# Optimization experiments

Measured on AMD Instinct MI355X. Metric: run time of the kernel, lower is better.

## Reference

```python
import jax, jax.numpy as jnp
import numpy as np
import math

HEADS = 4
LN_EPS = 1e-5


def _layer_norm(x, gamma, beta):
    # LayerNorm over last dim (N=4096), matching nn.LayerNorm(4096)
    mu = jnp.mean(x, axis=-1, keepdims=True)
    var = jnp.mean((x - mu) ** 2, axis=-1, keepdims=True)
    return (x - mu) * jax.lax.rsqrt(var + LN_EPS) * gamma + beta


def setup_inputs() -> dict:
    key = jax.random.key(0)
    ks = jax.random.split(key, 10)
    L, IMG, N = 1024, 1024, 4096
    s_img = 1.0 / math.sqrt(IMG)
    s_L = 1.0 / math.sqrt(L)
    return {
        "point_features": jax.random.normal(ks[0], (1, L, N), jnp.float32),
        "img_features": jax.random.normal(ks[1], (1, IMG, N), jnp.float32),
        # 4 per-head 1x1 convs IMG_chl -> L_chl
        "W_img": jax.random.normal(ks[2], (HEADS, L, IMG), jnp.float32) * s_img,
        "b_img": jax.random.normal(ks[3], (HEADS, L), jnp.float32) * s_img,
        # conv_L: L_chl -> L_chl
        "W_L": jax.random.normal(ks[4], (L, L), jnp.float32) * s_L,
        "b_L": jax.random.normal(ks[5], (L,), jnp.float32) * s_L,
        # LayerNorm(4096)
        "ln_g": jnp.ones((N,), jnp.float32),
        "ln_b": jnp.zeros((N,), jnp.float32),
        # conv_fusion: L_chl -> L_chl
        "W_f": jax.random.normal(ks[6], (L, L), jnp.float32) * s_L,
        "b_f": jax.random.normal(ks[7], (L,), jnp.float32) * s_L,
    }


def reference(point_features, img_features, W_img, b_img, W_L, b_L, ln_g, ln_b, W_f, b_f):
    # L_query = conv_L(point_features): [1, L, N]
    L_query = jnp.einsum('oi,bin->bon', W_L, point_features) + b_L[None, :, None]
    dk = L_query.shape[1]
    N = L_query.shape[2]

    # All 4 head keys at once: [H, 1, L, N]
    keys = jnp.einsum('hoi,bin->hbon', W_img, img_features) + b_img[:, None, :, None]

    # score_i = sum_c(key_i * query) / sqrt(dk)  -> cat over heads: [H, N] (B=1)
    score = jnp.sum(keys * L_query[None], axis=2).reshape(HEADS, N) / jnp.sqrt(jnp.float32(dk))

    # softmax across heads (dim=0), weightmap = [1, H, N]
    weight = jax.nn.softmax(score, axis=0)
    weightmap = weight[None]

    # z = sum_h weight[h] * key_h : [1, L, N]
    z = jnp.einsum('hn,hbcn->bcn', weight, keys)

    fused = _layer_norm(z + L_query, ln_g, ln_b)
    fusion_features = jnp.einsum('oi,bin->bon', W_f, fused) + b_f[None, :, None]
    return (fusion_features, weightmap)
```

## Files before the change

### kernel.cpp

```cpp
#include <hip/hip_runtime.h>
#include <hip/hip_bf16.h>
#include <stdint.h>

using u16 = unsigned short;

typedef __attribute__((ext_vector_type(8))) short bf16x8;
typedef __attribute__((ext_vector_type(4))) float f32x4;

typedef const __attribute__((address_space(1))) unsigned int* gas_t;
typedef __attribute__((address_space(3))) unsigned int* las_t;

__device__ inline void g2l16(const u16* g, u16* l) {
  __builtin_amdgcn_global_load_lds((gas_t)g, (las_t)l, 16, 0, 0);
}

__device__ inline u16 f2b(float x) {
  union { float f; uint32_t u; } v; v.f = x;
  uint32_t r = (v.u + 0x7FFFu + ((v.u >> 16) & 1u)) >> 16;
  return (u16)r;
}
__device__ inline float b2f(u16 b) {
  union { uint32_t u; float f; } v; v.u = ((uint32_t)b) << 16;
  return v.f;
}
__device__ inline float b2f_lo(uint32_t p) {
  union { uint32_t u; float f; } v; v.u = p << 16; return v.f;
}
__device__ inline float b2f_hi(uint32_t p) {
  union { uint32_t u; float f; } v; v.u = p & 0xFFFF0000u; return v.f;
}

__device__ inline void store_out(float* p, float v) { *p = v; }
__device__ inline void store_out(u16* p, float v) { *p = f2b(v); }

template<typename OutT>
__device__ inline void gemm_tile_128(const u16* __restrict__ A,
                                     const u16* __restrict__ Bt,
                                     const float* __restrict__ bias,
                                     OutT* __restrict__ C,
                                     int m0, int n0, int N, int K,
                                     u16* As, u16* Bs)
{
  const int tid  = threadIdx.x;
  const int wave = tid >> 6;
  const int lane = tid & 63;
  const int wm = wave >> 1, wn = wave & 1;
  const int lr = lane & 15;
  const int lq = lane >> 4;
  const int x7 = lr & 7;

  const int srow = tid >> 3;
  const int sgc  = (tid & 7) ^ (srow & 7);
  const u16* gA = A  + (size_t)(m0 + srow) * K + sgc * 8;
  const u16* gB = Bt + (size_t)(n0 + srow) * K + sgc * 8;
  u16* dstA = As + wave * 512;
  u16* dstB = Bs + wave * 512;

  f32x4 acc[4][4];
  #pragma unroll
  for (int i = 0; i < 4; ++i)
    #pragma unroll
    for (int j = 0; j < 4; ++j)
      acc[i][j] = (f32x4){0.f, 0.f, 0.f, 0.f};

  for (int k0 = 0; k0 < K; k0 += 64) {
    #pragma unroll
    for (int s = 0; s < 4; ++s) {
      g2l16(gA + (size_t)(s * 32) * K + k0, dstA + s * 2048);
      g2l16(gB + (size_t)(s * 32) * K + k0, dstB + s * 2048);
    }
    __syncthreads();

    #pragma unroll
    for (int ks = 0; ks < 2; ++ks) {
      const int pa = (ks * 4 + lq) ^ x7;
      bf16x8 af[4], bfr[4];
      #pragma unroll
      for (int im = 0; im < 4; ++im)
        af[im] = *(const bf16x8*)&As[(wm * 64 + im * 16 + lr) * 64 + pa * 8];
      #pragma unroll
      for (int in = 0; in < 4; ++in)
        bfr[in] = *(const bf16x8*)&Bs[(wn * 64 + in * 16 + lr) * 64 + pa * 8];

      #pragma unroll
      for (int im = 0; im < 4; ++im)
        #pragma unroll
        for (int in = 0; in < 4; ++in)
          acc[im][in] = __builtin_amdgcn_mfma_f32_16x16x32_bf16(
              af[im], bfr[in], acc[im][in], 0, 0, 0);
    }
    __syncthreads();
  }

  #pragma unroll
  for (int im = 0; im < 4; ++im) {
    const int mbase = m0 + wm * 64 + im * 16 + lq * 4;
    #pragma unroll
    for (int in = 0; in < 4; ++in) {
      const int ncol = n0 + wn * 64 + in * 16 + lr;
      #pragma unroll
      for (int r = 0; r < 4; ++r) {
        const int m = mbase + r;
        store_out(C + (size_t)m * N + ncol, acc[im][in][r] + bias[m]);
      }
    }
  }
}

__global__ __launch_bounds__(256)
void gemm_keys_q(const u16* __restrict__ WIb, const u16* __restrict__ IT,
                 const float* __restrict__ bim, u16* __restrict__ KEYS,
                 const u16* __restrict__ WLb, const u16* __restrict__ PT,
                 const float* __restrict__ bL, u16* __restrict__ Qb)
{
  __shared__ u16 As[128 * 64];
  __shared__ u16 Bs[128 * 64];
  const int by = blockIdx.y;
  const bool keys = (by < 32);
  const u16*   A    = keys ? WIb : WLb;
  const u16*   Bt   = keys ? IT  : PT;
  const float* bias = keys ? bim : bL;
  u16*         C    = keys ? KEYS : Qb;
  const int m0 = (by & 31) * 128;
  const int n0 = blockIdx.x * 128;
  gemm_tile_128<u16>(A, Bt, bias, C, m0, n0, 4096, 1024, As, Bs);
}

template<typename OutT>
__global__ __launch_bounds__(256)
void gemm_bt_64(const u16* __restrict__ A, const u16* __restrict__ Bt,
                const float* __restrict__ bias, OutT* __restrict__ C,
                int M, int N, int K)
{
  __shared__ u16 As[64 * 64];
  __shared__ u16 Bs[128 * 64];

  const int tid  = threadIdx.x;
  const int wave = tid >> 6;
  const int lane = tid & 63;
  const int lr = lane & 15;
  const int lq = lane >> 4;
  const int x7 = lr & 7;

  const int m0 = blockIdx.y * 64;
  const int n0 = blockIdx.x * 128;

  const int srow = tid >> 3;
  const int sgc  = (tid & 7) ^ (srow & 7);
  const u16* gA = A  + (size_t)(m0 + srow) * K + sgc * 8;
  const u16* gB = Bt + (size_t)(n0 + srow) * K + sgc * 8;
  u16* dstA = As + wave * 512;
  u16* dstB = Bs + wave * 512;

  f32x4 acc[4][2];
  #pragma unroll
  for (int i = 0; i < 4; ++i)
    #pragma unroll
    for (int j = 0; j < 2; ++j)
      acc[i][j] = (f32x4){0.f, 0.f, 0.f, 0.f};

  for (int k0 = 0; k0 < K; k0 += 64) {
    #pragma unroll
    for (int s = 0; s < 2; ++s)
      g2l16(gA + (size_t)(s * 32) * K + k0, dstA + s * 2048);
    #pragma unroll
    for (int s = 0; s < 4; ++s)
      g2l16(gB + (size_t)(s * 32) * K + k0, dstB + s * 2048);
    __syncthreads();

    #pragma unroll
    for (int ks = 0; ks < 2; ++ks) {
      const int pa = (ks * 4 + lq) ^ x7;
      bf16x8 af[4], bfr[2];
      #pragma unroll
      for (int im = 0; im < 4; ++im)
        af[im] = *(const bf16x8*)&As[(im * 16 + lr) * 64 + pa * 8];
      #pragma unroll
      for (int in = 0; in < 2; ++in)
        bfr[in] = *(const bf16x8*)&Bs[(wave * 32 + in * 16 + lr) * 64 + pa * 8];

      #pragma unroll
      for (int im = 0; im < 4; ++im)
        #pragma unroll
        for (int in = 0; in < 2; ++in)
          acc[im][in] = __builtin_amdgcn_mfma_f32_16x16x32_bf16(
              af[im], bfr[in], acc[im][in], 0, 0, 0);
    }
    __syncthreads();
  }

  #pragma unroll
  for (int im = 0; im < 4; ++im) {
    const int mbase = m0 + im * 16 + lq * 4;
    #pragma unroll
    for (int in = 0; in < 2; ++in) {
      const int ncol = n0 + wave * 32 + in * 16 + lr;
      #pragma unroll
      for (int r = 0; r < 4; ++r) {
        const int m = mbase + r;
        store_out(C + (size_t)m * N + ncol, acc[im][in][r] + bias[m]);
      }
    }
  }
}

__global__ __launch_bounds__(256)
void prep(const float* __restrict__ P, u16* __restrict__ PT,
          const float* __restrict__ I, u16* __restrict__ IT,
          const float4* __restrict__ wim, const float4* __restrict__ wl,
          const float4* __restrict__ wf, ushort4* __restrict__ wimb,
          ushort4* __restrict__ wlb, ushort4* __restrict__ wfb)
{
  const int bid = blockIdx.x;
  if (bid < 8192) {
    const int z   = bid >> 12;
    const int rem = bid & 4095;
    const int bx  = rem & 127;
    const int byy = rem >> 7;
    const float* in = z ? I : P;
    u16* out = z ? IT : PT;
    __shared__ u16 tile[32][33];
    const int c0 = bx * 32, r0 = byy * 32;
    const int tx = threadIdx.x & 31, ty = threadIdx.x >> 5;
    #pragma unroll
    for (int k = 0; k < 4; ++k)
      tile[ty + 8 * k][tx] = f2b(in[(size_t)(r0 + ty + 8 * k) * 4096 + c0 + tx]);
    __syncthreads();
    #pragma unroll
    for (int k = 0; k < 4; ++k)
      out[(size_t)(c0 + ty + 8 * k) * 1024 + r0 + tx] = tile[tx][ty + 8 * k];
  } else {
    int i = (bid - 8192) * 256 + threadIdx.x;
    const float4* src; ushort4* dst;
    if (i < 1048576)      { src = wim; dst = wimb; }
    else if (i < 1310720) { src = wl;  dst = wlb;  i -= 1048576; }
    else                  { src = wf;  dst = wfb;  i -= 1310720; }
    const float4 v = src[i];
    ushort4 o;
    o.x = f2b(v.x); o.y = f2b(v.y); o.z = f2b(v.z); o.w = f2b(v.w);
    dst[i] = o;
  }
}

__global__ __launch_bounds__(256)
void transpose_u16(const u16* __restrict__ in, u16* __restrict__ out,
                   int R, int C)
{
  __shared__ u16 tile[32][33];
  const int c0 = blockIdx.x * 32, r0 = blockIdx.y * 32;
  const int tx = threadIdx.x & 31, ty = threadIdx.x >> 5;
  #pragma unroll
  for (int k = 0; k < 4; ++k)
    tile[ty + 8 * k][tx] = in[(size_t)(r0 + ty + 8 * k) * C + c0 + tx];
  __syncthreads();
  #pragma unroll
  for (int k = 0; k < 4; ++k)
    out[(size_t)(c0 + ty + 8 * k) * R + r0 + tx] = tile[tx][ty + 8 * k];
}

__global__ __launch_bounds__(256)
void score_partial(const u16* __restrict__ keys, const u16* __restrict__ Qb,
                   float* __restrict__ score)
{
  const int n  = blockIdx.x * 256 + threadIdx.x;
  const int c0 = blockIdx.y * 32;
  float s[4] = {0.f, 0.f, 0.f, 0.f};
  for (int c = c0; c < c0 + 32; ++c) {
    const float q = b2f(Qb[(size_t)c * 4096 + n]);
    #pragma unroll
    for (int h = 0; h < 4; ++h)
      s[h] = fmaf(q, b2f(keys[((size_t)((h << 10) + c)) * 4096 + n]), s[h]);
  }
  #pragma unroll
  for (int h = 0; h < 4; ++h)
    atomicAdd(&score[h * 4096 + n], s[h] * 0.03125f);
}

__global__ __launch_bounds__(256)
void softmax_h(const float* __restrict__ score, float* __restrict__ wmap)
{
  const int n = blockIdx.x * 256 + threadIdx.x;
  const float s0 = score[n], s1 = score[4096 + n];
  const float s2 = score[8192 + n], s3 = score[12288 + n];
  const float m = fmaxf(fmaxf(s0, s1), fmaxf(s2, s3));
  const float e0 = expf(s0 - m), e1 = expf(s1 - m);
  const float e2 = expf(s2 - m), e3 = expf(s3 - m);
  const float inv = 1.f / (e0 + e1 + e2 + e3);
  wmap[n] = e0 * inv; wmap[4096 + n] = e1 * inv;
  wmap[8192 + n] = e2 * inv; wmap[12288 + n] = e3 * inv;
}

__global__ __launch_bounds__(256)
void z_ln(const u16* __restrict__ keys, const u16* __restrict__ Qb,
          const float* __restrict__ w, const float* __restrict__ g,
          const float* __restrict__ bb, u16* __restrict__ fused)
{
  const int c  = blockIdx.x;
  const int tx = threadIdx.x;
  float t[16];
  float s = 0.f, s2 = 0.f;
  #pragma unroll
  for (int j = 0; j < 2; ++j) {
    const int n = tx * 8 + j * 2048;
    const uint4 qv = *(const uint4*)&Qb[(size_t)c * 4096 + n];
    float z[8] = {0.f,0.f,0.f,0.f,0.f,0.f,0.f,0.f};
    #pragma unroll
    for (int h = 0; h < 4; ++h) {
      const uint4 kv = *(const uint4*)&keys[((size_t)((h << 10) + c)) * 4096 + n];
      const float4 w0 = *(const float4*)&w[h * 4096 + n];
      const float4 w1 = *(const float4*)&w[h * 4096 + n + 4];
      z[0] = fmaf(w0.x, b2f_lo(kv.x), z[0]);
      z[1] = fmaf(w0.y, b2f_hi(kv.x), z[1]);
      z[2] = fmaf(w0.z, b2f_lo(kv.y), z[2]);
      z[3] = fmaf(w0.w, b2f_hi(kv.y), z[3]);
      z[4] = fmaf(w1.x, b2f_lo(kv.z), z[4]);
      z[5] = fmaf(w1.y, b2f_hi(kv.z), z[5]);
      z[6] = fmaf(w1.z, b2f_lo(kv.w), z[6]);
      z[7] = fmaf(w1.w, b2f_hi(kv.w), z[7]);
    }
    const uint32_t qs[4] = {qv.x, qv.y, qv.z, qv.w};
    #pragma unroll
    for (int e = 0; e < 4; ++e) {
      const float v0 = z[2 * e]     + b2f_lo(qs[e]);
      const float v1 = z[2 * e + 1] + b2f_hi(qs[e]);
      t[8 * j + 2 * e]     = v0;
      t[8 * j + 2 * e + 1] = v1;
      s += v0 + v1;
      s2 = fmaf(v0, v0, fmaf(v1, v1, s2));
    }
  }
  #pragma unroll
  for (int o = 32; o > 0; o >>= 1) {
    s  += __shfl_down(s, o);
    s2 += __shfl_down(s2, o);
  }
  __shared__ float rbuf[8];
  const int wave = tx >> 6, lane = tx & 63;
  if (lane == 0) { rbuf[wave] = s; rbuf[4 + wave] = s2; }
  __syncthreads();
  s  = rbuf[0] + rbuf[1] + rbuf[2] + rbuf[3];
  s2 = rbuf[4] + rbuf[5] + rbuf[6] + rbuf[7];
  const float mu  = s * (1.f / 4096.f);
  const float var = s2 * (1.f / 4096.f) - mu * mu;
  const float rs  = rsqrtf(var + 1e-5f);
  #pragma unroll
  for (int j = 0; j < 2; ++j) {
    const int n = tx * 8 + j * 2048;
    #pragma unroll
    for (int q4 = 0; q4 < 2; ++q4) {
      const float4 gv = *(const float4*)&g[n + 4 * q4];
      const float4 bv = *(const float4*)&bb[n + 4 * q4];
      ushort4 o;
      o.x = f2b((t[8 * j + 4 * q4]     - mu) * rs * gv.x + bv.x);
      o.y = f2b((t[8 * j + 4 * q4 + 1] - mu) * rs * gv.y + bv.y);
      o.z = f2b((t[8 * j + 4 * q4 + 2] - mu) * rs * gv.z + bv.z);
      o.w = f2b((t[8 * j + 4 * q4 + 3] - mu) * rs * gv.w + bv.w);
      *(ushort4*)&fused[(size_t)c * 4096 + n + 4 * q4] = o;
    }
  }
}

extern "C" void kernel_launch(void* const* d_in, const int* in_sizes, int n_in,
                              void* d_out, int out_size, void* d_ws, size_t ws_size,
                              hipStream_t stream)
{
  const float* P   = (const float*)d_in[0];
  const float* I   = (const float*)d_in[1];
  const float* Wim = (const float*)d_in[2];
  const float* bim = (const float*)d_in[3];
  const float* WL  = (const float*)d_in[4];
  const float* bL  = (const float*)d_in[5];
  const float* lng = (const float*)d_in[6];
  const float* lnb = (const float*)d_in[7];
  const float* Wf  = (const float*)d_in[8];
  const float* bf_ = (const float*)d_in[9];
  float* out = (float*)d_out;

  char* ws = (char*)d_ws;
  u16*   PT     = (u16*)(ws + 0);
  u16*   IT     = (u16*)(ws + (size_t)8  * 1048576);
  u16*   WLb    = (u16*)(ws + (size_t)16 * 1048576);
  u16*   WIb    = (u16*)(ws + (size_t)18 * 1048576);
  u16*   WFb    = (u16*)(ws + (size_t)26 * 1048576);
  u16*   Qb     = (u16*)(ws + (size_t)28 * 1048576);
  u16*   KEYS   = (u16*)(ws + (size_t)36 * 1048576);
  float* SCORE  = (float*)(ws + (size_t)68 * 1048576);
  u16*   FUSED  = (u16*)(ws + (size_t)70 * 1048576);
  u16*   FUSEDT = (u16*)(ws + (size_t)78 * 1048576);

  const dim3 b256(256);

  prep<<<14336, b256, 0, stream>>>(P, PT, I, IT,
                                   (const float4*)Wim, (const float4*)WL,
                                   (const float4*)Wf, (ushort4*)WIb,
                                   (ushort4*)WLb, (ushort4*)WFb);

  gemm_keys_q<<<dim3(32, 40), b256, 0, stream>>>(WIb, IT, bim, KEYS,
                                                 WLb, PT, bL, Qb);

  hipMemsetAsync(SCORE, 0, 4 * 4096 * sizeof(float), stream);
  score_partial<<<dim3(16, 32), b256, 0, stream>>>(KEYS, Qb, SCORE);
  float* wmap = out + (size_t)1024 * 4096;
  softmax_h<<<16, b256, 0, stream>>>(SCORE, wmap);

  z_ln<<<1024, b256, 0, stream>>>(KEYS, Qb, wmap, lng, lnb, FUSED);
  transpose_u16<<<dim3(128, 32), b256, 0, stream>>>(FUSED, FUSEDT, 1024, 4096);

  gemm_bt_64<float><<<dim3(32, 16), b256, 0, stream>>>(WFb, FUSEDT, bf_, out, 1024, 4096, 1024);
}
```

Before: 212.6 us.

## Vectorize transposes with 64x64 tiles and replace score atomics with partial sums

The fp32->bf16 input transposes and the fused-output transpose now use 64x64 LDS tiles with vector loads and stores instead of 32x32 scalar accesses. The score reduction writes per-channel-block partial sums into a reused workspace region rather than doing atomicAdd onto a memset buffer. The softmax kernel sums the 64 partials. This removes the memset and the atomic contention but adds an extra 4MB partial-buffer read in softmax.

```diff
diff --git a/kernel.cpp b/kernel.cpp
--- a/kernel.cpp
+++ b/kernel.cpp
@@ -212,25 +212,38 @@
           ushort4* __restrict__ wlb, ushort4* __restrict__ wfb)
 {
   const int bid = blockIdx.x;
-  if (bid < 8192) {
-    const int z   = bid >> 12;
-    const int rem = bid & 4095;
-    const int bx  = rem & 127;
-    const int byy = rem >> 7;
+  if (bid < 2048) {
+    const int z   = bid >> 10;
+    const int rem = bid & 1023;
+    const int ct  = rem & 63;
+    const int rt  = rem >> 6;
     const float* in = z ? I : P;
     u16* out = z ? IT : PT;
-    __shared__ u16 tile[32][33];
-    const int c0 = bx * 32, r0 = byy * 32;
-    const int tx = threadIdx.x & 31, ty = threadIdx.x >> 5;
-    #pragma unroll
-    for (int k = 0; k < 4; ++k)
-      tile[ty + 8 * k][tx] = f2b(in[(size_t)(r0 + ty + 8 * k) * 4096 + c0 + tx]);
+    __shared__ u16 tile[64][72];
+    const int r0 = rt * 64, c0 = ct * 64;
+    const int tr  = threadIdx.x >> 4;
+    const int tc4 = threadIdx.x & 15;
+    #pragma unroll
+    for (int it = 0; it < 4; ++it) {
+      const int r = it * 16 + tr;
+      const float4 v = *(const float4*)&in[(size_t)(r0 + r) * 4096 + c0 + tc4 * 4];
+      ushort4 o;
+      o.x = f2b(v.x); o.y = f2b(v.y); o.z = f2b(v.z); o.w = f2b(v.w);
+      *(ushort4*)&tile[r][tc4 * 4] = o;
+    }
     __syncthreads();
     #pragma unroll
-    for (int k = 0; k < 4; ++k)
-      out[(size_t)(c0 + ty + 8 * k) * 1024 + r0 + tx] = tile[tx][ty + 8 * k];
+    for (int it = 0; it < 4; ++it) {
+      const int c = it * 16 + tr;
+      ushort4 o;
+      o.x = tile[tc4 * 4 + 0][c];
+      o.y = tile[tc4 * 4 + 1][c];
+      o.z = tile[tc4 * 4 + 2][c];
+      o.w = tile[tc4 * 4 + 3][c];
+      *(ushort4*)&out[(size_t)(c0 + c) * 1024 + r0 + tc4 * 4] = o;
+    }
   } else {
-    int i = (bid - 8192) * 256 + threadIdx.x;
+    int i = (bid - 2048) * 256 + threadIdx.x;
     const float4* src; ushort4* dst;
     if (i < 1048576)      { src = wim; dst = wimb; }
     else if (i < 1310720) { src = wl;  dst = wlb;  i -= 1048576; }
@@ -246,42 +259,73 @@
 void transpose_u16(const u16* __restrict__ in, u16* __restrict__ out,
                    int R, int C)
 {
-  __shared__ u16 tile[32][33];
-  const int c0 = blockIdx.x * 32, r0 = blockIdx.y * 32;
-  const int tx = threadIdx.x & 31, ty = threadIdx.x >> 5;
-  #pragma unroll
-  for (int k = 0; k < 4; ++k)
-    tile[ty + 8 * k][tx] = in[(size_t)(r0 + ty + 8 * k) * C + c0 + tx];
+  __shared__ u16 tile[64][72];
+  const int c0 = blockIdx.x * 64, r0 = blockIdx.y * 64;
+  const int tr  = threadIdx.x >> 4;
+  const int tc4 = threadIdx.x & 15;
+  #pragma unroll
+  for (int it = 0; it < 4; ++it) {
+    const int r = it * 16 + tr;
+    *(ushort4*)&tile[r][tc4 * 4] =
+        *(const ushort4*)&in[(size_t)(r0 + r) * C + c0 + tc4 * 4];
+  }
   __syncthreads();
   #pragma unroll
-  for (int k = 0; k < 4; ++k)
-    out[(size_t)(c0 + ty + 8 * k) * R + r0 + tx] = tile[tx][ty + 8 * k];
+  for (int it = 0; it < 4; ++it) {
+    const int c = it * 16 + tr;
+    ushort4 o;
+    o.x = tile[tc4 * 4 + 0][c];
+    o.y = tile[tc4 * 4 + 1][c];
+    o.z = tile[tc4 * 4 + 2][c];
+    o.w = tile[tc4 * 4 + 3][c];
+    *(ushort4*)&out[(size_t)(c0 + c) * R + r0 + tc4 * 4] = o;
+  }
 }
 
 __global__ __launch_bounds__(256)
 void score_partial(const u16* __restrict__ keys, const u16* __restrict__ Qb,
-                   float* __restrict__ score)
-{
-  const int n  = blockIdx.x * 256 + threadIdx.x;
-  const int c0 = blockIdx.y * 32;
-  float s[4] = {0.f, 0.f, 0.f, 0.f};
-  for (int c = c0; c < c0 + 32; ++c) {
-    const float q = b2f(Qb[(size_t)c * 4096 + n]);
-    #pragma unroll
-    for (int h = 0; h < 4; ++h)
-      s[h] = fmaf(q, b2f(keys[((size_t)((h << 10) + c)) * 4096 + n]), s[h]);
-  }
+                   float* __restrict__ part)
+{
+  const int n  = blockIdx.x * 1024 + threadIdx.x * 4;
+  const int c0 = blockIdx.y * 16;
+  float s[4][4];
   #pragma unroll
   for (int h = 0; h < 4; ++h)
-    atomicAdd(&score[h * 4096 + n], s[h] * 0.03125f);
-}
-
-__global__ __launch_bounds__(256)
-void softmax_h(const float* __restrict__ score, float* __restrict__ wmap)
+    #pragma unroll
+    for (int e = 0; e < 4; ++e) s[h][e] = 0.f;
+
+  for (int c = c0; c < c0 + 16; ++c) {
+    const uint2 qv = *(const uint2*)&Qb[(size_t)c * 4096 + n];
+    const float q0 = b2f_lo(qv.x), q1 = b2f_hi(qv.x);
+    const float q2 = b2f_lo(qv.y), q3 = b2f_hi(qv.y);
+    #pragma unroll
+    for (int h = 0; h < 4; ++h) {
+      const uint2 kv = *(const uint2*)&keys[((size_t)((h << 10) + c)) * 4096 + n];
+      s[h][0] = fmaf(q0, b2f_lo(kv.x), s[h][0]);
+      s[h][1] = fmaf(q1, b2f_hi(kv.x), s[h][1]);
+      s[h][2] = fmaf(q2, b2f_lo(kv.y), s[h][2]);
+      s[h][3] = fmaf(q3, b2f_hi(kv.y), s[h][3]);
+    }
+  }
+  #pragma unroll
+  for (int h = 0; h < 4; ++h) {
+    float4 o;
+    o.x = s[h][0] * 0.03125f; o.y = s[h][1] * 0.03125f;
+    o.z = s[h][2] * 0.03125f; o.w = s[h][3] * 0.03125f;
+    *(float4*)&part[((size_t)(blockIdx.y * 4 + h)) * 4096 + n] = o;
+  }
+}
+
+__global__ __launch_bounds__(256)
+void softmax_h(const float* __restrict__ part, float* __restrict__ wmap)
 {
   const int n = blockIdx.x * 256 + threadIdx.x;
-  const float s0 = score[n], s1 = score[4096 + n];
-  const float s2 = score[8192 + n], s3 = score[12288 + n];
+  float s0 = 0.f, s1 = 0.f, s2 = 0.f, s3 = 0.f;
+  #pragma unroll 4
+  for (int cy = 0; cy < 64; ++cy) {
+    const float* p = part + (size_t)cy * 16384 + n;
+    s0 += p[0]; s1 += p[4096]; s2 += p[8192]; s3 += p[12288];
+  }
   const float m = fmaxf(fmaxf(s0, s1), fmaxf(s2, s3));
   const float e0 = expf(s0 - m), e1 = expf(s1 - m);
   const float e2 = expf(s2 - m), e3 = expf(s3 - m);
@@ -384,27 +428,26 @@
   u16*   WFb    = (u16*)(ws + (size_t)26 * 1048576);
   u16*   Qb     = (u16*)(ws + (size_t)28 * 1048576);
   u16*   KEYS   = (u16*)(ws + (size_t)36 * 1048576);
-  float* SCORE  = (float*)(ws + (size_t)68 * 1048576);
+  float* PART   = (float*)(ws + 0);
   u16*   FUSED  = (u16*)(ws + (size_t)70 * 1048576);
   u16*   FUSEDT = (u16*)(ws + (size_t)78 * 1048576);
 
   const dim3 b256(256);
 
-  prep<<<14336, b256, 0, stream>>>(P, PT, I, IT,
-                                   (const float4*)Wim, (const float4*)WL,
-                                   (const float4*)Wf, (ushort4*)WIb,
-                                   (ushort4*)WLb, (ushort4*)WFb);
+  prep<<<8192, b256, 0, stream>>>(P, PT, I, IT,
+                                  (const float4*)Wim, (const float4*)WL,
+                                  (const float4*)Wf, (ushort4*)WIb,
+                                  (ushort4*)WLb, (ushort4*)WFb);
 
   gemm_keys_q<<<dim3(32, 40), b256, 0, stream>>>(WIb, IT, bim, KEYS,
                                                  WLb, PT, bL, Qb);
 
-  hipMemsetAsync(SCORE, 0, 4 * 4096 * sizeof(float), stream);
-  score_partial<<<dim3(16, 32), b256, 0, stream>>>(KEYS, Qb, SCORE);
+  score_partial<<<dim3(4, 64), b256, 0, stream>>>(KEYS, Qb, PART);
   float* wmap = out + (size_t)1024 * 4096;
-  softmax_h<<<16, b256, 0, stream>>>(SCORE, wmap);
+  softmax_h<<<16, b256, 0, stream>>>(PART, wmap);
 
   z_ln<<<1024, b256, 0, stream>>>(KEYS, Qb, wmap, lng, lnb, FUSED);
-  transpose_u16<<<dim3(128, 32), b256, 0, stream>>>(FUSED, FUSEDT, 1024, 4096);
+  transpose_u16<<<dim3(64, 16), b256, 0, stream>>>(FUSED, FUSEDT, 1024, 4096);
 
   gemm_bt_64<float><<<dim3(32, 16), b256, 0, stream>>>(WFb, FUSEDT, bf_, out, 1024, 4096, 1024);
 }
```

Measured after the change: 217.8 us. +2.4%, slower.

## Fuse score reduction into key GEMM epilogue, compute query GEMM separately first

Applied to the files above, without the earlier changes.

The query projection now runs first as its own GEMM launch, so the key GEMM epilogue can read the query tile and build the per-head score partial sums directly. The partials are reduced across lanes with shuffles and added atomically. This removes the separate score kernel and its full re-read of the keys tensor. In exchange the query and key GEMMs no longer share one launch, the epilogue does extra global loads of the query values, and there are more atomics on the score buffer.

```diff
diff --git a/kernel.cpp b/kernel.cpp
--- a/kernel.cpp
+++ b/kernel.cpp
@@ -33,13 +33,10 @@
 __device__ inline void store_out(float* p, float v) { *p = v; }
 __device__ inline void store_out(u16* p, float v) { *p = f2b(v); }
 
-template<typename OutT>
-__device__ inline void gemm_tile_128(const u16* __restrict__ A,
+__device__ inline void gemm_core_128(const u16* __restrict__ A,
                                      const u16* __restrict__ Bt,
-                                     const float* __restrict__ bias,
-                                     OutT* __restrict__ C,
-                                     int m0, int n0, int N, int K,
-                                     u16* As, u16* Bs)
+                                     int m0, int n0, int K,
+                                     u16* As, u16* Bs, f32x4 (&acc)[4][4])
 {
   const int tid  = threadIdx.x;
   const int wave = tid >> 6;
@@ -56,7 +53,6 @@
   u16* dstA = As + wave * 512;
   u16* dstB = Bs + wave * 512;
 
-  f32x4 acc[4][4];
   #pragma unroll
   for (int i = 0; i < 4; ++i)
     #pragma unroll
@@ -91,7 +87,29 @@
     }
     __syncthreads();
   }
-
+}
+
+__global__ __launch_bounds__(256)
+void gemm_keys_score(const u16* __restrict__ WIb, const u16* __restrict__ IT,
+                     const float* __restrict__ bim, u16* __restrict__ KEYS,
+                     const u16* __restrict__ Qb, float* __restrict__ score)
+{
+  __shared__ u16 As[128 * 64];
+  __shared__ u16 Bs[128 * 64];
+  const int m0 = blockIdx.y * 128;
+  const int n0 = blockIdx.x * 128;
+  f32x4 acc[4][4];
+  gemm_core_128(WIb, IT, m0, n0, 1024, As, Bs, acc);
+
+  const int tid  = threadIdx.x;
+  const int wave = tid >> 6;
+  const int lane = tid & 63;
+  const int wm = wave >> 1, wn = wave & 1;
+  const int lr = lane & 15;
+  const int lq = lane >> 4;
+  const int h  = m0 >> 10;
+
+  float sp[4] = {0.f, 0.f, 0.f, 0.f};
   #pragma unroll
   for (int im = 0; im < 4; ++im) {
     const int mbase = m0 + wm * 64 + im * 16 + lq * 4;
@@ -101,29 +119,21 @@
       #pragma unroll
       for (int r = 0; r < 4; ++r) {
         const int m = mbase + r;
-        store_out(C + (size_t)m * N + ncol, acc[im][in][r] + bias[m]);
+        const float v = acc[im][in][r] + bim[m];
+        KEYS[(size_t)m * 4096 + ncol] = f2b(v);
+        sp[in] = fmaf(v, b2f(Qb[(size_t)(m & 1023) * 4096 + ncol]), sp[in]);
       }
     }
   }
-}
-
-__global__ __launch_bounds__(256)
-void gemm_keys_q(const u16* __restrict__ WIb, const u16* __restrict__ IT,
-                 const float* __restrict__ bim, u16* __restrict__ KEYS,
-                 const u16* __restrict__ WLb, const u16* __restrict__ PT,
-                 const float* __restrict__ bL, u16* __restrict__ Qb)
-{
-  __shared__ u16 As[128 * 64];
-  __shared__ u16 Bs[128 * 64];
-  const int by = blockIdx.y;
-  const bool keys = (by < 32);
-  const u16*   A    = keys ? WIb : WLb;
-  const u16*   Bt   = keys ? IT  : PT;
-  const float* bias = keys ? bim : bL;
-  u16*         C    = keys ? KEYS : Qb;
-  const int m0 = (by & 31) * 128;
-  const int n0 = blockIdx.x * 128;
-  gemm_tile_128<u16>(A, Bt, bias, C, m0, n0, 4096, 1024, As, Bs);
+  #pragma unroll
+  for (int in = 0; in < 4; ++in) {
+    float v = sp[in];
+    v += __shfl_down(v, 32);
+    v += __shfl_down(v, 16);
+    if (lane < 16)
+      atomicAdd(&score[h * 4096 + n0 + wn * 64 + in * 16 + lane],
+                v * 0.03125f);
+  }
 }
 
 template<typename OutT>
@@ -259,24 +269,6 @@
 }
 
 __global__ __launch_bounds__(256)
-void score_partial(const u16* __restrict__ keys, const u16* __restrict__ Qb,
-                   float* __restrict__ score)
-{
-  const int n  = blockIdx.x * 256 + threadIdx.x;
-  const int c0 = blockIdx.y * 32;
-  float s[4] = {0.f, 0.f, 0.f, 0.f};
-  for (int c = c0; c < c0 + 32; ++c) {
-    const float q = b2f(Qb[(size_t)c * 4096 + n]);
-    #pragma unroll
-    for (int h = 0; h < 4; ++h)
-      s[h] = fmaf(q, b2f(keys[((size_t)((h << 10) + c)) * 4096 + n]), s[h]);
-  }
-  #pragma unroll
-  for (int h = 0; h < 4; ++h)
-    atomicAdd(&score[h * 4096 + n], s[h] * 0.03125f);
-}
-
-__global__ __launch_bounds__(256)
 void softmax_h(const float* __restrict__ score, float* __restrict__ wmap)
 {
   const int n = blockIdx.x * 256 + threadIdx.x;
@@ -395,16 +387,19 @@
                                    (const float4*)Wf, (ushort4*)WIb,
                                    (ushort4*)WLb, (ushort4*)WFb);
 
-  gemm_keys_q<<<dim3(32, 40), b256, 0, stream>>>(WIb, IT, bim, KEYS,
-                                                 WLb, PT, bL, Qb);
+  gemm_bt_64<u16><<<dim3(32, 16), b256, 0, stream>>>(WLb, PT, bL, Qb,
+                                                     1024, 4096, 1024);
 
   hipMemsetAsync(SCORE, 0, 4 * 4096 * sizeof(float), stream);
-  score_partial<<<dim3(16, 32), b256, 0, stream>>>(KEYS, Qb, SCORE);
+  gemm_keys_score<<<dim3(32, 32), b256, 0, stream>>>(WIb, IT, bim, KEYS,
+                                                     Qb, SCORE);
+
   float* wmap = out + (size_t)1024 * 4096;
   softmax_h<<<16, b256, 0, stream>>>(SCORE, wmap);
 
   z_ln<<<1024, b256, 0, stream>>>(KEYS, Qb, wmap, lng, lnb, FUSED);
   transpose_u16<<<dim3(128, 32), b256, 0, stream>>>(FUSED, FUSEDT, 1024, 4096);
 
-  gemm_bt_64<float><<<dim3(32, 16), b256, 0, stream>>>(WFb, FUSEDT, bf_, out, 1024, 4096, 1024);
-}
+  gemm_bt_64<float><<<dim3(32, 16), b256, 0, stream>>>(WFb, FUSEDT, bf_, out,
+                                                       1024, 4096, 1024);
+}
```

Result: no change. 208.9 us (-1.7%).
